# Kernel tuning notes

Measured on AMD Instinct MI355X. Metric: run time of the kernel, lower is better.

Reference implementation:

```python
import jax, jax.numpy as jnp
import numpy as np

B, P, ENC = 64, 196, 2048
ATT, DEC, EMB = 512, 512, 512
V, MAXLEN = 10000, 30


def setup_inputs() -> dict:
    key = jax.random.key(0)
    ks = jax.random.split(key, 20)
    s = 0.02
    inp = {
        "encoder_out": jax.random.normal(ks[0], (B, P, ENC), jnp.float32),
        "captions": jax.random.randint(ks[1], (B, MAXLEN), 0, V).astype(jnp.int64),
        "caption_lengths": jax.random.randint(ks[2], (B,), 1, MAXLEN).astype(jnp.int64),
        # parameters (PyTorch Linear convention: y = x @ W.T + b)
        "emb_table": jax.random.uniform(ks[3], (V, EMB), jnp.float32, -0.1, 0.1),
        "W_enc_att": jax.random.normal(ks[4], (ATT, ENC), jnp.float32) * s,
        "b_enc_att": jnp.zeros((ATT,), jnp.float32),
        "W_dec_att": jax.random.normal(ks[5], (ATT, DEC), jnp.float32) * s,
        "b_dec_att": jnp.zeros((ATT,), jnp.float32),
        "w_full_att": jax.random.normal(ks[6], (1, ATT), jnp.float32) * s,
        "b_full_att": jnp.zeros((1,), jnp.float32),
        "W_ih": jax.random.normal(ks[7], (4 * DEC, EMB + ENC), jnp.float32) * s,
        "b_ih": jnp.zeros((4 * DEC,), jnp.float32),
        "W_hh": jax.random.normal(ks[8], (4 * DEC, DEC), jnp.float32) * s,
        "b_hh": jnp.zeros((4 * DEC,), jnp.float32),
        "W_init_h": jax.random.normal(ks[9], (DEC, ENC), jnp.float32) * s,
        "b_init_h": jnp.zeros((DEC,), jnp.float32),
        "W_init_c": jax.random.normal(ks[10], (DEC, ENC), jnp.float32) * s,
        "b_init_c": jnp.zeros((DEC,), jnp.float32),
        "W_fc": jax.random.uniform(ks[11], (V, DEC), jnp.float32, -0.1, 0.1),
        "b_fc": jnp.zeros((V,), jnp.float32),
    }
    return inp


def reference(encoder_out, captions, caption_lengths, emb_table,
              W_enc_att, b_enc_att, W_dec_att, b_dec_att,
              w_full_att, b_full_att, W_ih, b_ih, W_hh, b_hh,
              W_init_h, b_init_h, W_init_c, b_init_c, W_fc, b_fc):
    # init hidden state from mean-pooled encoder features
    mean_enc = encoder_out.mean(axis=1)                       # [B, ENC]
    h0 = mean_enc @ W_init_h.T + b_init_h                     # [B, DEC]
    c0 = mean_enc @ W_init_c.T + b_init_c                     # [B, DEC]

    # encoder-side attention projection is time-invariant: hoist out of the loop
    att1 = jnp.einsum('bpe,ae->bpa', encoder_out, W_enc_att) + b_enc_att  # [B, P, ATT]

    embeddings = emb_table[captions]                          # [B, T, EMB]
    T = captions.shape[1] - 1
    emb_steps = jnp.swapaxes(embeddings[:, :T, :], 0, 1)      # [T, B, EMB]

    def step(carry, emb_t):
        h, c = carry
        att2 = h @ W_dec_att.T + b_dec_att                    # [B, ATT]
        e = (jax.nn.relu(att1 + att2[:, None, :]) @ w_full_att.T + b_full_att)[..., 0]  # [B, P]
        alpha = jax.nn.softmax(e, axis=1)                     # [B, P]
        context = jnp.einsum('bp,bpe->be', alpha, encoder_out)  # [B, ENC]
        x = jnp.concatenate([emb_t, context], axis=1)         # [B, EMB+ENC]
        gates = x @ W_ih.T + b_ih + h @ W_hh.T + b_hh         # [B, 4*DEC]
        i, f, g, o = jnp.split(gates, 4, axis=1)
        c_new = jax.nn.sigmoid(f) * c + jax.nn.sigmoid(i) * jnp.tanh(g)
        h_new = jax.nn.sigmoid(o) * jnp.tanh(c_new)
        preds = h_new @ W_fc.T + b_fc                         # dropout in eval mode = identity
        return (h_new, c_new), (preds, alpha)

    _, (preds_seq, alpha_seq) = jax.lax.scan(step, (h0, c0), emb_steps)
    predictions = jnp.swapaxes(preds_seq, 0, 1)               # [B, T, V]
    alphas = jnp.swapaxes(alpha_seq, 0, 1)                    # [B, T, P]
    return predictions, alphas
```

## Files before the change

### kernel.cpp

```cpp
#include <hip/hip_runtime.h>
#include <cstddef>

constexpr int B_   = 64;
constexpr int P_   = 196;
constexpr int ENC_ = 2048;
constexpr int ATT_ = 512;
constexpr int DEC_ = 512;
constexpr int EMB_ = 512;
constexpr int V_   = 10000;
constexpr int MAXLEN_ = 30;
constexpr int T_   = 29;
constexpr int G4_  = 2048;
constexpr int KIH_ = 2560;
constexpr int XK2_ = 2560;

constexpr int NBLK = 256;
constexpr int TPB  = 1024;
constexpr int NT   = NBLK * TPB;
constexpr int NW   = NT / 64;
constexpr int FSTR = 16;
constexpr size_t ZS_ = (size_t)B_ * G4_;
constexpr int NPT = 625;

typedef __attribute__((ext_vector_type(8))) short short8;
typedef __attribute__((ext_vector_type(4))) float f32x4;
using us = unsigned short;

__device__ __forceinline__ us f2bf(float x) {
    union { float f; unsigned u; } v; v.f = x;
    unsigned r = v.u + 0x7fff + ((v.u >> 16) & 1);
    return (us)(r >> 16);
}
__device__ __forceinline__ float bf2f(us u) {
    union { unsigned u; float f; } v; v.u = ((unsigned)u) << 16;
    return v.f;
}

__device__ __forceinline__ unsigned ld4cc(const void* p) {
    unsigned r;
    asm volatile("global_load_dword %0, %1, off sc1\n\ts_waitcnt vmcnt(0)"
                 : "=v"(r) : "v"(p) : "memory");
    return r;
}
__device__ __forceinline__ void ld4cc_x8(const float* p0, const float* p1,
                                         const float* p2, const float* p3,
                                         const float* p4, const float* p5,
                                         const float* p6, const float* p7,
                                         float* o) {
    float r0, r1, r2, r3, r4, r5, r6, r7;
    asm volatile("global_load_dword %0, %8, off sc1\n\t"
                 "global_load_dword %1, %9, off sc1\n\t"
                 "global_load_dword %2, %10, off sc1\n\t"
                 "global_load_dword %3, %11, off sc1\n\t"
                 "global_load_dword %4, %12, off sc1\n\t"
                 "global_load_dword %5, %13, off sc1\n\t"
                 "global_load_dword %6, %14, off sc1\n\t"
                 "global_load_dword %7, %15, off sc1\n\t"
                 "s_waitcnt vmcnt(0)"
                 : "=&v"(r0), "=&v"(r1), "=&v"(r2), "=&v"(r3),
                   "=&v"(r4), "=&v"(r5), "=&v"(r6), "=&v"(r7)
                 : "v"(p0), "v"(p1), "v"(p2), "v"(p3),
                   "v"(p4), "v"(p5), "v"(p6), "v"(p7) : "memory");
    o[0]=r0; o[1]=r1; o[2]=r2; o[3]=r3; o[4]=r4; o[5]=r5; o[6]=r6; o[7]=r7;
}
__device__ __forceinline__ void ld16cc_x3(const void* p0, const void* p1, const void* p2,
                                          short8* a, short8* b, short8* c) {
    short8 ra, rb, rc;
    asm volatile("global_load_dwordx4 %0, %3, off sc1\n\t"
                 "global_load_dwordx4 %1, %4, off sc1\n\t"
                 "global_load_dwordx4 %2, %5, off sc1\n\t"
                 "s_waitcnt vmcnt(0)"
                 : "=&v"(ra), "=&v"(rb), "=&v"(rc)
                 : "v"(p0), "v"(p1), "v"(p2) : "memory");
    *a = ra; *b = rb; *c = rc;
}
__device__ __forceinline__ void ld16cc_x4(const void* p0, const void* p1,
                                          const void* p2, const void* p3,
                                          short8* a, short8* b, short8* c, short8* d) {
    short8 ra, rb, rc, rd;
    asm volatile("global_load_dwordx4 %0, %4, off sc1\n\t"
                 "global_load_dwordx4 %1, %5, off sc1\n\t"
                 "global_load_dwordx4 %2, %6, off sc1\n\t"
                 "global_load_dwordx4 %3, %7, off sc1\n\t"
                 "s_waitcnt vmcnt(0)"
                 : "=&v"(ra), "=&v"(rb), "=&v"(rc), "=&v"(rd)
                 : "v"(p0), "v"(p1), "v"(p2), "v"(p3) : "memory");
    *a = ra; *b = rb; *c = rc; *d = rd;
}
__device__ __forceinline__ void ldf8cc(const void* p0, const void* p1, f32x4* a, f32x4* b) {
    f32x4 ra, rb;
    asm volatile("global_load_dwordx4 %0, %2, off sc1\n\t"
                 "global_load_dwordx4 %1, %3, off sc1\n\t"
                 "s_waitcnt vmcnt(0)"
                 : "=&v"(ra), "=&v"(rb) : "v"(p0), "v"(p1) : "memory");
    *a = ra; *b = rb;
}
__device__ __forceinline__ void st4cc(void* p, unsigned v) {
    asm volatile("global_store_dword %0, %1, off sc1" :: "v"(p), "v"(v) : "memory");
}
__device__ __forceinline__ void st2cc(void* p, unsigned v) {
    asm volatile("global_store_short %0, %1, off sc1" :: "v"(p), "v"(v) : "memory");
}
__device__ __forceinline__ float wredsum(float a) {
#pragma unroll
    for (int o = 32; o > 0; o >>= 1) a += __shfl_xor(a, o);
    return a;
}

template<bool REL>
__device__ __forceinline__ void gbar_arrive(unsigned* flags, unsigned tok) {
    asm volatile("s_waitcnt vmcnt(0)" ::: "memory");
    __syncthreads();
    if (threadIdx.x == 0)
        __hip_atomic_store(&flags[blockIdx.x * FSTR], tok,
                           REL ? __ATOMIC_RELEASE : __ATOMIC_RELAXED,
                           __HIP_MEMORY_SCOPE_AGENT);
}
__device__ __forceinline__ void gbar_wait(unsigned* flags, unsigned tok) {
    if (threadIdx.x < NBLK) {
        while (__hip_atomic_load(&flags[threadIdx.x * FSTR], __ATOMIC_RELAXED,
                                 __HIP_MEMORY_SCOPE_AGENT) < tok)
            __builtin_amdgcn_s_sleep(1);
    }
    __syncthreads();
}
template<bool REL>
__device__ __forceinline__ void gbar(unsigned* flags, unsigned tok) {
    gbar_arrive<REL>(flags, tok);
    gbar_wait(flags, tok);
}

__device__ __forceinline__ void cvt8(const float* __restrict__ src, us* __restrict__ dst) {
    const float4* p = (const float4*)src;
    float4 a = p[0], b = p[1];
    union { short8 v; us u[8]; } o;
    o.u[0] = f2bf(a.x); o.u[1] = f2bf(a.y); o.u[2] = f2bf(a.z); o.u[3] = f2bf(a.w);
    o.u[4] = f2bf(b.x); o.u[5] = f2bf(b.y); o.u[6] = f2bf(b.z); o.u[7] = f2bf(b.w);
    *(short8*)dst = o.v;
}

__device__ __forceinline__ float score8(short8 v, const f32x4& lo, const f32x4& hi,
                                        const float4& w0, const float4& w1) {
    float acc = 0.f, x;
    x = bf2f((us)v[0]) + lo[0]; acc += fmaxf(x, 0.f) * w0.x;
    x = bf2f((us)v[1]) + lo[1]; acc += fmaxf(x, 0.f) * w0.y;
    x = bf2f((us)v[2]) + lo[2]; acc += fmaxf(x, 0.f) * w0.z;
    x = bf2f((us)v[3]) + lo[3]; acc += fmaxf(x, 0.f) * w0.w;
    x = bf2f((us)v[4]) + hi[0]; acc += fmaxf(x, 0.f) * w1.x;
    x = bf2f((us)v[5]) + hi[1]; acc += fmaxf(x, 0.f) * w1.y;
    x = bf2f((us)v[6]) + hi[2]; acc += fmaxf(x, 0.f) * w1.z;
    x = bf2f((us)v[7]) + hi[3]; acc += fmaxf(x, 0.f) * w1.w;
    return acc;
}

__device__ __forceinline__ void preds_task(const us* s_h, const us* __restrict__ wfcb,
                                           const float* __restrict__ b_fc,
                                           float* __restrict__ outp,
                                           int nt, int tt, int lane) {
    const int r = lane & 15, g = lane >> 4;
    f32x4 acc[4] = {{0,0,0,0},{0,0,0,0},{0,0,0,0},{0,0,0,0}};
    const us* Brow = wfcb + (size_t)(nt*16 + r)*DEC_ + g*8;
    const us* As   = s_h + r*520 + g*8;
#pragma unroll
    for (int k0 = 0; k0 < DEC_; k0 += 64) {
        short8 b0 = *(const short8*)(Brow + k0);
        short8 b1 = *(const short8*)(Brow + k0 + 32);
#pragma unroll
        for (int mt = 0; mt < 4; ++mt) {
            short8 a0 = *(const short8*)(As + mt*16*520 + k0);
            short8 a1 = *(const short8*)(As + mt*16*520 + k0 + 32);
            acc[mt] = __builtin_amdgcn_mfma_f32_16x16x32_bf16(a0, b0, acc[mt], 0, 0, 0);
            acc[mt] = __builtin_amdgcn_mfma_f32_16x16x32_bf16(a1, b1, acc[mt], 0, 0, 0);
        }
    }
    const int n = nt*16 + r;
    const float bv = b_fc[n];
#pragma unroll
    for (int mt = 0; mt < 4; ++mt)
#pragma unroll
        for (int i = 0; i < 4; ++i) {
            int b = mt*16 + g*4 + i;
            outp[(size_t)b*(T_*V_) + (size_t)tt*V_ + n] = acc[mt][i] + bv;
        }
}

__global__ __launch_bounds__(TPB) void k_persist(
    const float* __restrict__ enc, const int* __restrict__ captions,
    const float* __restrict__ emb_table,
    const float* __restrict__ W_enc_att, const float* __restrict__ b_enc_att,
    const float* __restrict__ W_dec_att, const float* __restrict__ b_dec_att,
    const float* __restrict__ w_full,
    const float* __restrict__ W_ih, const float* __restrict__ b_ih,
    const float* __restrict__ W_hh, const float* __restrict__ b_hh,
    const float* __restrict__ W_init_h, const float* __restrict__ b_init_h,
    const float* __restrict__ W_init_c, const float* __restrict__ b_init_c,
    const float* __restrict__ W_fc, const float* __restrict__ b_fc,
    us* encb, us* wencb, us* wdecb, us* wfcb, us* wcat2, us* wembW,
    us* winitb, us* xembA, us* att1b, us* hbuf, us* xcatb, us* meanbb,
    float* cst, float* att2G, float* gp, float* gpe, float* bsum,
    unsigned* flags, float* outp, float* outa)
{
    __shared__ us s_stage[64 * 520];
    __shared__ us s_wb[64 * 328];
    __shared__ us s_wd[16 * 520];
    __shared__ float s_e[P_];
    __shared__ float s_al[P_];
    __shared__ float s_red[32];

    const int tid = threadIdx.x, bid = blockIdx.x;
    const int gtid = bid * TPB + tid;
    const int wid  = gtid >> 6;
    const int w    = tid >> 6;
    const int lane = tid & 63;
    unsigned tok = 0;
    float creg = 0.f;
    us* const hb0 = hbuf;
    us* const hb1 = hbuf + (size_t)B_ * DEC_;

    for (int i = gtid; i < B_*P_*ENC_/8; i += NT) cvt8(enc + (size_t)i*8, encb + (size_t)i*8);
    for (int i = gtid; i < ATT_*ENC_/8; i += NT) cvt8(W_enc_att + (size_t)i*8, wencb + (size_t)i*8);
    for (int i = gtid; i < ATT_*DEC_/8; i += NT) cvt8(W_dec_att + (size_t)i*8, wdecb + (size_t)i*8);
    for (int i = gtid; i < V_*DEC_/8;   i += NT) cvt8(W_fc + (size_t)i*8, wfcb + (size_t)i*8);
    for (int i = gtid; i < G4_*XK2_/8;  i += NT) {
        int n = (i*8) / XK2_, k = (i*8) % XK2_;
        const float* src = (k < ENC_) ? (W_ih + (size_t)n*KIH_ + EMB_ + k)
                                      : (W_hh + (size_t)n*DEC_ + (k - ENC_));
        cvt8(src, wcat2 + (size_t)i*8);
    }
    for (int i = gtid; i < G4_*EMB_/8;  i += NT)
        cvt8(W_ih + ((size_t)((i*8) / EMB_))*KIH_ + ((i*8) % EMB_), wembW + (size_t)i*8);
    for (int i = gtid; i < 1024*ENC_/8; i += NT) {
        int n = (i*8) >> 11, k = (i*8) & (ENC_ - 1);
        const float* src = (n < 512) ? (W_init_h + (size_t)n*ENC_ + k)
                                     : (W_init_c + (size_t)(n-512)*ENC_ + k);
        cvt8(src, winitb + (size_t)i*8);
    }
    for (int i = gtid; i < T_*B_*EMB_/8; i += NT) {
        int r = i >> 6, c8 = i & 63;
        int t = r >> 6, b = r & 63;
        int cap = captions[b*MAXLEN_ + t];
        cvt8(emb_table + (size_t)cap*EMB_ + c8*8, xembA + (size_t)r*EMB_ + c8*8);
    }
    if (gtid < G4_) bsum[gtid] = b_ih[gtid] + b_hh[gtid];
    if (gtid < B_*ENC_) {
        int b = gtid >> 11, e = gtid & (ENC_ - 1);
        const float* base = enc + (size_t)b*P_*ENC_ + e;
        float s = 0.f;
        for (int p = 0; p < P_; ++p) s += base[(size_t)p*ENC_];
        meanbb[gtid] = f2bf(s * (1.f / P_));
    }
    gbar<true>(flags, ++tok);

    for (int task = wid; task < 256 + 1856; task += NW) {
        const int r = lane & 15, g = lane >> 4;
        if (task < 256) {
            const int mt = task & 3, nt = task >> 2;
            const int m0 = mt*16, n0 = nt*16;
            const us* Ar = meanbb + (size_t)(m0 + r)*ENC_ + g*8;
            const us* Br = winitb + (size_t)(n0 + r)*ENC_ + g*8;
            f32x4 acc0 = {0,0,0,0}, acc1 = {0,0,0,0};
#pragma unroll 4
            for (int k0 = 0; k0 < ENC_; k0 += 64) {
                acc0 = __builtin_amdgcn_mfma_f32_16x16x32_bf16(
                    *(const short8*)(Ar + k0), *(const short8*)(Br + k0), acc0, 0, 0, 0);
                acc1 = __builtin_amdgcn_mfma_f32_16x16x32_bf16(
                    *(const short8*)(Ar + k0 + 32), *(const short8*)(Br + k0 + 32), acc1, 0, 0, 0);
            }
            const int n = n0 + r;
            if (n < 512) {
                float bv = b_init_h[n];
#pragma unroll
                for (int i = 0; i < 4; ++i) {
                    int b = m0 + g*4 + i;
                    unsigned hv = f2bf(acc0[i] + acc1[i] + bv);
                    st2cc(hb1 + b*DEC_ + n, hv);
                    st2cc(xcatb + (size_t)b*XK2_ + ENC_ + n, hv);
                }
            } else {
                int d = n - 512;
                float bv = b_init_c[d];
#pragma unroll
                for (int i = 0; i < 4; ++i)
                    st4cc(cst + (m0 + g*4 + i)*DEC_ + d,
                          __float_as_uint(acc0[i] + acc1[i] + bv));
            }
        } else {
            const int q = task - 256;
            const int m0 = (q >> 6) * 64, n0 = (q & 63) * 32;
            f32x4 acc[4][2] = {};
            const us* Ab = xembA + (size_t)(m0 + r)*EMB_ + g*8;
            const us* Bb = wembW + (size_t)(n0 + r)*EMB_ + g*8;
#pragma unroll 2
            for (int k0 = 0; k0 < EMB_; k0 += 32) {
                short8 af[4], bfr[2];
#pragma unroll
                for (int mi = 0; mi < 4; ++mi)
                    af[mi] = *(const short8*)(Ab + (size_t)mi*16*EMB_ + k0);
#pragma unroll
                for (int nj = 0; nj < 2; ++nj)
                    bfr[nj] = *(const short8*)(Bb + (size_t)nj*16*EMB_ + k0);
#pragma unroll
                for (int mi = 0; mi < 4; ++mi)
#pragma unroll
                    for (int nj = 0; nj < 2; ++nj)
                        acc[mi][nj] = __builtin_amdgcn_mfma_f32_16x16x32_bf16(
                            af[mi], bfr[nj], acc[mi][nj], 0, 0, 0);
            }
#pragma unroll
            for (int mi = 0; mi < 4; ++mi)
#pragma unroll
                for (int nj = 0; nj < 2; ++nj) {
                    int n = n0 + nj*16 + r;
                    float bv = bsum[n];
#pragma unroll
                    for (int i = 0; i < 4; ++i) {
                        int m = m0 + mi*16 + g*4 + i;
                        gpe[(size_t)m*G4_ + n] = acc[mi][nj][i] + bv;
                    }
                }
        }
    }
    gbar<true>(flags, ++tok);

    for (int task = wid; task < 3264; task += NW) {
        const int r = lane & 15, g = lane >> 4;
        if (task < 3136) {
            int mt = task >> 4, nt2 = task & 15;
            int m0 = mt*64, n0 = nt2*32;
            f32x4 acc[4][2] = {};
            const us* Ab = encb + (size_t)(m0 + r)*ENC_ + g*8;
            const us* Bb = wencb + (size_t)(n0 + r)*ENC_ + g*8;
#pragma unroll 2
            for (int k0 = 0; k0 < ENC_; k0 += 32) {
                short8 af[4], bfr[2];
#pragma unroll
                for (int mi = 0; mi < 4; ++mi)
                    af[mi] = *(const short8*)(Ab + (size_t)mi*16*ENC_ + k0);
#pragma unroll
                for (int nj = 0; nj < 2; ++nj)
                    bfr[nj] = *(const short8*)(Bb + (size_t)nj*16*ENC_ + k0);
#pragma unroll
                for (int mi = 0; mi < 4; ++mi)
#pragma unroll
                    for (int nj = 0; nj < 2; ++nj)
                        acc[mi][nj] = __builtin_amdgcn_mfma_f32_16x16x32_bf16(
                            af[mi], bfr[nj], acc[mi][nj], 0, 0, 0);
            }
#pragma unroll
            for (int mi = 0; mi < 4; ++mi)
#pragma unroll
                for (int nj = 0; nj < 2; ++nj) {
                    int n = n0 + nj*16 + r;
                    float bv = b_enc_att[n];
#pragma unroll
                    for (int i = 0; i < 4; ++i) {
                        int m = m0 + mi*16 + g*4 + i;
                        att1b[(size_t)m*ATT_ + n] = f2bf(acc[mi][nj][i] + bv);
                    }
                }
        } else {
            int q = task - 3136;
            int nt = q >> 2, mt = q & 3;
            const us* Ar = hb1 + (size_t)(mt*16 + r)*DEC_ + g*8;
            const us* Br = wdecb + (size_t)(nt*16 + r)*DEC_ + g*8;
            f32x4 acc0 = {0,0,0,0}, acc1 = {0,0,0,0};
#pragma unroll 4
            for (int k0 = 0; k0 < DEC_; k0 += 64) {
                short8 a0, a1, dum;
                ld16cc_x3(Ar + k0, Ar + k0 + 32, Ar + k0, &a0, &a1, &dum);
                acc0 = __builtin_amdgcn_mfma_f32_16x16x32_bf16(
                    a0, *(const short8*)(Br + k0), acc0, 0, 0, 0);
                acc1 = __builtin_amdgcn_mfma_f32_16x16x32_bf16(
                    a1, *(const short8*)(Br + k0 + 32), acc1, 0, 0, 0);
            }
            int n = nt*16 + r;
            float bv = b_dec_att[n];
#pragma unroll
            for (int i = 0; i < 4; ++i)
                st4cc(att2G + (size_t)(mt*16 + g*4 + i)*ATT_ + n,
                      __float_as_uint(acc0[i] + acc1[i] + bv));
        }
    }
    gbar<true>(flags, ++tok);

    {
        const int z = bid >> 5, nb = bid & 31;
        for (int c = tid; c < 2560; c += TPB) {
            int row = c / 40, col8 = c % 40;
            *(short8*)(s_wb + row*328 + col8*8) =
                *(const short8*)(wcat2 + (size_t)(nb*64 + row)*XK2_ + (size_t)z*320 + col8*8);
        }
        if (bid < 32)
            for (int c = tid; c < 1024; c += TPB) {
                int row = c >> 6, col8 = c & 63;
                *(short8*)(s_wd + row*520 + col8*8) =
                    *(const short8*)(wdecb + (size_t)(bid*16 + row)*DEC_ + col8*8);
            }
        if (tid < 128) creg = __uint_as_float(ld4cc(cst + bid*128 + tid));
        __syncthreads();
    }

    for (int t = 0; t < T_; ++t) {
        {
            const int b = bid & 63, cc = bid >> 6;
            f32x4 a2lo, a2hi;
            const float* ap = att2G + (size_t)b*ATT_ + lane*8;
            ldf8cc(ap, ap + 4, &a2lo, &a2hi);
            const float4 w0 = *(const float4*)(w_full + lane*8);
            const float4 w1 = *(const float4*)(w_full + lane*8 + 4);
            const us* a1base = att1b + (size_t)b*P_*ATT_ + lane*8;
            for (int p = w; p < P_; p += 32) {
                const int p2 = p + 16;
                short8 v0 = *(const short8*)(a1base + (size_t)p*ATT_);
                short8 v1 = (p2 < P_) ? *(const short8*)(a1base + (size_t)p2*ATT_) : v0;
                float acc0 = score8(v0, a2lo, a2hi, w0, w1);
                float acc1 = score8(v1, a2lo, a2hi, w0, w1);
                acc0 = wredsum(acc0);
                acc1 = wredsum(acc1);
                if (lane == 0) {
                    s_e[p] = acc0;
                    if (p2 < P_) s_e[p2] = acc1;
                }
            }
            __syncthreads();
            float v = (tid < P_) ? s_e[tid] : -3.4e38f;
            float mx = v;
#pragma unroll
            for (int o = 32; o > 0; o >>= 1) mx = fmaxf(mx, __shfl_xor(mx, o));
            if (lane == 0) s_red[w] = mx;
            __syncthreads();
            mx = s_red[0];
#pragma unroll
            for (int j = 1; j < 16; ++j) mx = fmaxf(mx, s_red[j]);
            float ev = (tid < P_) ? expf(v - mx) : 0.f;
            float sm = wredsum(ev);
            if (lane == 0) s_red[16 + w] = sm;
            __syncthreads();
            float tot = 0.f;
#pragma unroll
            for (int j = 0; j < 16; ++j) tot += s_red[16 + j];
            if (tid < P_) {
                float al = ev / tot;
                s_al[tid] = al;
                if (cc == 0) outa[((size_t)b*T_ + t)*P_ + tid] = al;
            }
            __syncthreads();
            float a[8] = {};
            const us* ep = encb + (size_t)b*P_*ENC_ + cc*512 + lane*8;
            for (int p = w; p < P_; p += 16) {
                short8 vv = *(const short8*)(ep + (size_t)p*ENC_);
                float al = s_al[p];
#pragma unroll
                for (int j = 0; j < 8; ++j) a[j] += al * bf2f((us)vv[j]);
            }
            float* s_accf = (float*)s_stage;
            {
                f32x4 lo = {a[0],a[1],a[2],a[3]}, hi = {a[4],a[5],a[6],a[7]};
                *(f32x4*)(s_accf + w*512 + lane*8)     = lo;
                *(f32x4*)(s_accf + w*512 + lane*8 + 4) = hi;
            }
            __syncthreads();
            if (tid < 256) {
                int c2 = tid*2;
                float s0 = 0.f, s1 = 0.f;
#pragma unroll
                for (int q = 0; q < 16; ++q) {
                    s0 += s_accf[q*512 + c2];
                    s1 += s_accf[q*512 + c2 + 1];
                }
                unsigned pk = (unsigned)f2bf(s0) | ((unsigned)f2bf(s1) << 16);
                st4cc(xcatb + (size_t)b*XK2_ + cc*512 + c2, pk);
            }
            __syncthreads();
        }
        gbar<false>(flags, ++tok);

        {
            const int z = bid >> 5;
            {
                short8 v0, v1, v2;
                int c0 = tid, c1 = tid + 1024, c2i = tid + 2048;
                const us* p0 = xcatb + (size_t)(c0/40)*XK2_ + z*320 + (c0%40)*8;
                const us* p1 = xcatb + (size_t)(c1/40)*XK2_ + z*320 + (c1%40)*8;
                bool has2 = c2i < 2560;
                const us* p2 = has2 ? xcatb + (size_t)(c2i/40)*XK2_ + z*320 + (c2i%40)*8 : p0;
                ld16cc_x3(p0, p1, p2, &v0, &v1, &v2);
                *(short8*)(s_stage + (c0/40)*328 + (c0%40)*8) = v0;
                *(short8*)(s_stage + (c1/40)*328 + (c1%40)*8) = v1;
                if (has2) *(short8*)(s_stage + (c2i/40)*328 + (c2i%40)*8) = v2;
            }
            __syncthreads();
            const int nt = (bid & 31)*4 + (w >> 2), mt = w & 3;
            const int r = lane & 15, g = lane >> 4;
            const us* sxr = s_stage + (mt*16 + r)*328 + g*8;
            const us* Br  = s_wb + ((w >> 2)*16 + r)*328 + g*8;
            f32x4 acc0 = {0,0,0,0}, acc1 = {0,0,0,0};
#pragma unroll
            for (int k0 = 0; k0 < 320; k0 += 64) {
                acc0 = __builtin_amdgcn_mfma_f32_16x16x32_bf16(
                    *(const short8*)(sxr + k0), *(const short8*)(Br + k0), acc0, 0, 0, 0);
                acc1 = __builtin_amdgcn_mfma_f32_16x16x32_bf16(
                    *(const short8*)(sxr + k0 + 32), *(const short8*)(Br + k0 + 32), acc1, 0, 0, 0);
            }
            const int n = nt*16 + r;
#pragma unroll
            for (int i = 0; i < 4; ++i) {
                int m = mt*16 + g*4 + i;
                st4cc(gp + ZS_*z + (size_t)m*G4_ + n, __float_as_uint(acc0[i] + acc1[i]));
            }
            __syncthreads();
        }
        gbar<false>(flags, ++tok);

        {
            float* sg = (float*)s_stage;
            if (tid < 512) {
                const int cell = tid & 127, gate = tid >> 7;
                const int idx = bid*128 + cell;
                const int b = idx >> 9, d = idx & 511;
                const float* gz = gp + (size_t)b*G4_ + gate*512 + d;
                float vz[8];
                ld4cc_x8(gz, gz + ZS_, gz + 2*ZS_, gz + 3*ZS_,
                         gz + 4*ZS_, gz + 5*ZS_, gz + 6*ZS_, gz + 7*ZS_, vz);
                sg[tid] = ((vz[0]+vz[1]) + (vz[2]+vz[3])) + ((vz[4]+vz[5]) + (vz[6]+vz[7]));
            }
            __syncthreads();
            if (tid < 128) {
                const int idx = bid*128 + tid;
                const int b = idx >> 9, d = idx & 511;
                const float* ge = gpe + ((size_t)(t*B_ + b))*G4_ + d;
                float gi = sg[tid]       + ge[0];
                float gf = sg[128 + tid] + ge[512];
                float gg = sg[256 + tid] + ge[1024];
                float go = sg[384 + tid] + ge[1536];
                float si = 1.f / (1.f + expf(-gi));
                float sf = 1.f / (1.f + expf(-gf));
                float so = 1.f / (1.f + expf(-go));
                float cn = sf * creg + si * tanhf(gg);
                creg = cn;
                float hn = so * tanhf(cn);
                unsigned hv = f2bf(hn);
                us* hnew = (t & 1) ? hb1 : hb0;
                st2cc(hnew + idx, hv);
                st2cc(xcatb + (size_t)b*XK2_ + ENC_ + d, hv);
            }
        }
        gbar<false>(flags, ++tok);

        if (t != T_ - 1) {
            ++tok;
            if (bid < 32) {
                {
                    const us* hbn = (t & 1) ? hb1 : hb0;
                    short8 v0, v1, v2, v3;
                    int c0 = tid, c1 = tid + 1024, c2i = tid + 2048, c3 = tid + 3072;
                    ld16cc_x4(hbn + (c0>>6)*DEC_ + (c0&63)*8, hbn + (c1>>6)*DEC_ + (c1&63)*8,
                              hbn + (c2i>>6)*DEC_ + (c2i&63)*8, hbn + (c3>>6)*DEC_ + (c3&63)*8,
                              &v0, &v1, &v2, &v3);
                    *(short8*)(s_stage + (c0>>6)*520 + (c0&63)*8) = v0;
                    *(short8*)(s_stage + (c1>>6)*520 + (c1&63)*8) = v1;
                    *(short8*)(s_stage + (c2i>>6)*520 + (c2i&63)*8) = v2;
                    *(short8*)(s_stage + (c3>>6)*520 + (c3&63)*8) = v3;
                }
                __syncthreads();
                if (w < 4) {
                    const int r = lane & 15, g = lane >> 4;
                    const us* As = s_stage + (w*16 + r)*520 + g*8;
                    const us* Bs = s_wd + r*520 + g*8;
                    f32x4 acc0 = {0,0,0,0}, acc1 = {0,0,0,0};
#pragma unroll
                    for (int k0 = 0; k0 < DEC_; k0 += 64) {
                        acc0 = __builtin_amdgcn_mfma_f32_16x16x32_bf16(
                            *(const short8*)(As + k0), *(const short8*)(Bs + k0), acc0, 0, 0, 0);
                        acc1 = __builtin_amdgcn_mfma_f32_16x16x32_bf16(
                            *(const short8*)(As + k0 + 32), *(const short8*)(Bs + k0 + 32), acc1, 0, 0, 0);
                    }
                    const int n = bid*16 + r;
                    float bv = b_dec_att[n];
#pragma unroll
                    for (int i = 0; i < 4; ++i)
                        st4cc(att2G + (size_t)(w*16 + g*4 + i)*ATT_ + n,
                              __float_as_uint(acc0[i] + acc1[i] + bv));
                }
                gbar_arrive<false>(flags, tok);
                gbar_wait(flags, tok);
            } else {
                gbar_arrive<false>(flags, tok);
                if (t > 0) {
                    const us* hbo = (t & 1) ? hb0 : hb1;
                    short8 v0, v1, v2, v3;
                    int c0 = tid, c1 = tid + 1024, c2i = tid + 2048, c3 = tid + 3072;
                    ld16cc_x4(hbo + (c0>>6)*DEC_ + (c0&63)*8, hbo + (c1>>6)*DEC_ + (c1&63)*8,
                              hbo + (c2i>>6)*DEC_ + (c2i&63)*8, hbo + (c3>>6)*DEC_ + (c3&63)*8,
                              &v0, &v1, &v2, &v3);
                    *(short8*)(s_stage + (c0>>6)*520 + (c0&63)*8) = v0;
                    *(short8*)(s_stage + (c1>>6)*520 + (c1&63)*8) = v1;
                    *(short8*)(s_stage + (c2i>>6)*520 + (c2i&63)*8) = v2;
                    *(short8*)(s_stage + (c3>>6)*520 + (c3&63)*8) = v3;
                    __syncthreads();
                    const int tq = (bid - 32)*3 + w;
                    if (w < 3 && tq < NPT)
                        preds_task(s_stage, wfcb, b_fc, outp, tq, t - 1, lane);
                }
                gbar_wait(flags, tok);
            }
        } else {
            if (bid >= 32) {
                const us* hbo = (t & 1) ? hb0 : hb1;
                short8 v0, v1, v2, v3;
                int c0 = tid, c1 = tid + 1024, c2i = tid + 2048, c3 = tid + 3072;
                ld16cc_x4(hbo + (c0>>6)*DEC_ + (c0&63)*8, hbo + (c1>>6)*DEC_ + (c1&63)*8,
                          hbo + (c2i>>6)*DEC_ + (c2i&63)*8, hbo + (c3>>6)*DEC_ + (c3&63)*8,
                          &v0, &v1, &v2, &v3);
                *(short8*)(s_stage + (c0>>6)*520 + (c0&63)*8) = v0;
                *(short8*)(s_stage + (c1>>6)*520 + (c1&63)*8) = v1;
                *(short8*)(s_stage + (c2i>>6)*520 + (c2i&63)*8) = v2;
                *(short8*)(s_stage + (c3>>6)*520 + (c3&63)*8) = v3;
                __syncthreads();
                const int tq = (bid - 32)*3 + w;
                if (w < 3 && tq < NPT)
                    preds_task(s_stage, wfcb, b_fc, outp, tq, t - 1, lane);
            }
        }
    }

    if (bid < 40) {
        __syncthreads();
        const us* hbn = ((T_ - 1) & 1) ? hb1 : hb0;
        {
            short8 v0, v1, v2, v3;
            int c0 = tid, c1 = tid + 1024, c2i = tid + 2048, c3 = tid + 3072;
            ld16cc_x4(hbn + (c0>>6)*DEC_ + (c0&63)*8, hbn + (c1>>6)*DEC_ + (c1&63)*8,
                      hbn + (c2i>>6)*DEC_ + (c2i&63)*8, hbn + (c3>>6)*DEC_ + (c3&63)*8,
                      &v0, &v1, &v2, &v3);
            *(short8*)(s_stage + (c0>>6)*520 + (c0&63)*8) = v0;
            *(short8*)(s_stage + (c1>>6)*520 + (c1&63)*8) = v1;
            *(short8*)(s_stage + (c2i>>6)*520 + (c2i&63)*8) = v2;
            *(short8*)(s_stage + (c3>>6)*520 + (c3&63)*8) = v3;
        }
        __syncthreads();
        const int tq = bid*16 + w;
        if (tq < NPT)
            preds_task(s_stage, wfcb, b_fc, outp, tq, T_ - 1, lane);
    }
}

extern "C" void kernel_launch(void* const* d_in, const int* in_sizes, int n_in,
                              void* d_out, int out_size, void* d_ws, size_t ws_size,
                              hipStream_t stream) {
    const float* enc       = (const float*)d_in[0];
    const int*   captions  = (const int*)d_in[1];
    const float* emb_table = (const float*)d_in[3];
    const float* W_enc_att = (const float*)d_in[4];
    const float* b_enc_att = (const float*)d_in[5];
    const float* W_dec_att = (const float*)d_in[6];
    const float* b_dec_att = (const float*)d_in[7];
    const float* w_full    = (const float*)d_in[8];
    const float* W_ih      = (const float*)d_in[10];
    const float* b_ih      = (const float*)d_in[11];
    const float* W_hh      = (const float*)d_in[12];
    const float* b_hh      = (const float*)d_in[13];
    const float* W_init_h  = (const float*)d_in[14];
    const float* b_init_h  = (const float*)d_in[15];
    const float* W_init_c  = (const float*)d_in[16];
    const float* b_init_c  = (const float*)d_in[17];
    const float* W_fc      = (const float*)d_in[18];
    const float* b_fc      = (const float*)d_in[19];

    char* ws = (char*)d_ws;
    size_t off = 0;
    auto alloc = [&](size_t bytes) {
        void* p = ws + off;
        off = (off + bytes + 255) & ~(size_t)255;
        return p;
    };
    us* encb   = (us*)alloc((size_t)B_ * P_ * ENC_ * 2);
    us* wencb  = (us*)alloc((size_t)ATT_ * ENC_ * 2);
    us* wdecb  = (us*)alloc((size_t)ATT_ * DEC_ * 2);
    us* wfcb   = (us*)alloc((size_t)V_ * DEC_ * 2);
    us* wcat2  = (us*)alloc((size_t)G4_ * XK2_ * 2);
    us* wembW  = (us*)alloc((size_t)G4_ * EMB_ * 2);
    us* winitb = (us*)alloc((size_t)1024 * ENC_ * 2);
    us* xembA  = (us*)alloc((size_t)T_ * B_ * EMB_ * 2);
    us* att1b  = (us*)alloc((size_t)B_ * P_ * ATT_ * 2);
    us* hbuf   = (us*)alloc((size_t)2 * B_ * DEC_ * 2);
    us* xcatb  = (us*)alloc((size_t)B_ * XK2_ * 2);
    us* meanbb = (us*)alloc((size_t)B_ * ENC_ * 2);
    float* cst   = (float*)alloc((size_t)B_ * DEC_ * 4);
    float* att2G = (float*)alloc((size_t)B_ * ATT_ * 4);
    float* gp    = (float*)alloc((size_t)B_ * G4_ * 8 * 4);
    float* gpe   = (float*)alloc((size_t)T_ * B_ * G4_ * 4);
    float* bsum  = (float*)alloc((size_t)G4_ * 4);
    unsigned* flags = (unsigned*)alloc((size_t)(NBLK + 1) * FSTR * 4);

    float* outp = (float*)d_out;
    float* outa = outp + (size_t)B_ * T_ * V_;

    hipMemsetAsync(flags, 0, (NBLK + 1) * FSTR * sizeof(unsigned), stream);
    k_persist<<<NBLK, TPB, 0, stream>>>(
        enc, captions, emb_table, W_enc_att, b_enc_att, W_dec_att, b_dec_att,
        w_full, W_ih, b_ih, W_hh, b_hh, W_init_h, b_init_h, W_init_c, b_init_c,
        W_fc, b_fc,
        encb, wencb, wdecb, wfcb, wcat2, wembW, winitb, xembA, att1b, hbuf, xcatb,
        meanbb, cst, att2G, gp, gpe, bsum, flags, outp, outa);
}
```

Measured before the change: 1.204 ms.

## Fuse LSTM gate GEMM with cell update per block, dropping a grid barrier

Reorders the gate-weight rows so each of 128 blocks owns 4 hidden units across all four gates over the full K. That lets a block finish its gate GEMM, reduce it through shared memory and apply the LSTM cell update without the global split-K partial buffer and its extra grid barrier. The prediction GEMM moves onto the other 128 blocks and runs concurrently with the gate step, so fewer blocks do the recurrent work. A-operands are now loaded straight from global memory into registers, and the full 16x2560 weight slice stays resident in LDS.

Measured after the change: 1.573 ms. 1.31x slower.

```diff
diff --git a/kernel.cpp b/kernel.cpp
--- a/kernel.cpp
+++ b/kernel.cpp
@@ -19,7 +19,6 @@
 constexpr int NT   = NBLK * TPB;
 constexpr int NW   = NT / 64;
 constexpr int FSTR = 16;
-constexpr size_t ZS_ = (size_t)B_ * G4_;
 constexpr int NPT = 625;
 
 typedef __attribute__((ext_vector_type(8))) short short8;
@@ -41,27 +40,6 @@
     asm volatile("global_load_dword %0, %1, off sc1\n\ts_waitcnt vmcnt(0)"
                  : "=v"(r) : "v"(p) : "memory");
     return r;
-}
-__device__ __forceinline__ void ld4cc_x8(const float* p0, const float* p1,
-                                         const float* p2, const float* p3,
-                                         const float* p4, const float* p5,
-                                         const float* p6, const float* p7,
-                                         float* o) {
-    float r0, r1, r2, r3, r4, r5, r6, r7;
-    asm volatile("global_load_dword %0, %8, off sc1\n\t"
-                 "global_load_dword %1, %9, off sc1\n\t"
-                 "global_load_dword %2, %10, off sc1\n\t"
-                 "global_load_dword %3, %11, off sc1\n\t"
-                 "global_load_dword %4, %12, off sc1\n\t"
-                 "global_load_dword %5, %13, off sc1\n\t"
-                 "global_load_dword %6, %14, off sc1\n\t"
-                 "global_load_dword %7, %15, off sc1\n\t"
-                 "s_waitcnt vmcnt(0)"
-                 : "=&v"(r0), "=&v"(r1), "=&v"(r2), "=&v"(r3),
-                   "=&v"(r4), "=&v"(r5), "=&v"(r6), "=&v"(r7)
-                 : "v"(p0), "v"(p1), "v"(p2), "v"(p3),
-                   "v"(p4), "v"(p5), "v"(p6), "v"(p7) : "memory");
-    o[0]=r0; o[1]=r1; o[2]=r2; o[3]=r3; o[4]=r4; o[5]=r5; o[6]=r6; o[7]=r7;
 }
 __device__ __forceinline__ void ld16cc_x3(const void* p0, const void* p1, const void* p2,
                                           short8* a, short8* b, short8* c) {
@@ -108,26 +86,19 @@
 }
 
 template<bool REL>
-__device__ __forceinline__ void gbar_arrive(unsigned* flags, unsigned tok) {
+__device__ __forceinline__ void gbar(unsigned* flags, unsigned tok) {
     asm volatile("s_waitcnt vmcnt(0)" ::: "memory");
     __syncthreads();
     if (threadIdx.x == 0)
         __hip_atomic_store(&flags[blockIdx.x * FSTR], tok,
                            REL ? __ATOMIC_RELEASE : __ATOMIC_RELAXED,
                            __HIP_MEMORY_SCOPE_AGENT);
-}
-__device__ __forceinline__ void gbar_wait(unsigned* flags, unsigned tok) {
     if (threadIdx.x < NBLK) {
         while (__hip_atomic_load(&flags[threadIdx.x * FSTR], __ATOMIC_RELAXED,
                                  __HIP_MEMORY_SCOPE_AGENT) < tok)
             __builtin_amdgcn_s_sleep(1);
     }
     __syncthreads();
-}
-template<bool REL>
-__device__ __forceinline__ void gbar(unsigned* flags, unsigned tok) {
-    gbar_arrive<REL>(flags, tok);
-    gbar_wait(flags, tok);
 }
 
 __device__ __forceinline__ void cvt8(const float* __restrict__ src, us* __restrict__ dst) {
@@ -197,12 +168,11 @@
     const float* __restrict__ W_fc, const float* __restrict__ b_fc,
     us* encb, us* wencb, us* wdecb, us* wfcb, us* wcat2, us* wembW,
     us* winitb, us* xembA, us* att1b, us* hbuf, us* xcatb, us* meanbb,
-    float* cst, float* att2G, float* gp, float* gpe, float* bsum,
+    float* cst, float* att2G, float* gpe, float* bsum,
     unsigned* flags, float* outp, float* outa)
 {
     __shared__ us s_stage[64 * 520];
-    __shared__ us s_wb[64 * 328];
-    __shared__ us s_wd[16 * 520];
+    __shared__ us s_w[16 * 2568];
     __shared__ float s_e[P_];
     __shared__ float s_al[P_];
     __shared__ float s_red[32];
@@ -222,7 +192,9 @@
     for (int i = gtid; i < ATT_*DEC_/8; i += NT) cvt8(W_dec_att + (size_t)i*8, wdecb + (size_t)i*8);
     for (int i = gtid; i < V_*DEC_/8;   i += NT) cvt8(W_fc + (size_t)i*8, wfcb + (size_t)i*8);
     for (int i = gtid; i < G4_*XK2_/8;  i += NT) {
-        int n = (i*8) / XK2_, k = (i*8) % XK2_;
+        int rr = (i*8) / XK2_, k = (i*8) % XK2_;
+        int j = rr & 15, kblk = rr >> 4;
+        int n = (j >> 2)*512 + kblk*4 + (j & 3);
         const float* src = (k < ENC_) ? (W_ih + (size_t)n*KIH_ + EMB_ + k)
                                       : (W_hh + (size_t)n*DEC_ + (k - ENC_));
         cvt8(src, wcat2 + (size_t)i*8);
@@ -383,22 +355,25 @@
     }
     gbar<true>(flags, ++tok);
 
-    {
-        const int z = bid >> 5, nb = bid & 31;
-        for (int c = tid; c < 2560; c += TPB) {
-            int row = c / 40, col8 = c % 40;
-            *(short8*)(s_wb + row*328 + col8*8) =
-                *(const short8*)(wcat2 + (size_t)(nb*64 + row)*XK2_ + (size_t)z*320 + col8*8);
-        }
-        if (bid < 32)
-            for (int c = tid; c < 1024; c += TPB) {
-                int row = c >> 6, col8 = c & 63;
-                *(short8*)(s_wd + row*520 + col8*8) =
-                    *(const short8*)(wdecb + (size_t)(bid*16 + row)*DEC_ + col8*8);
-            }
-        if (tid < 128) creg = __uint_as_float(ld4cc(cst + bid*128 + tid));
-        __syncthreads();
-    }
+    if (bid >= 128) {
+        const int kblk = bid - 128;
+        for (int c = tid; c < 16*320; c += TPB) {
+            int row = c / 320, col8 = c % 320;
+            *(short8*)(s_w + row*2568 + col8*8) =
+                *(const short8*)(wcat2 + (size_t)(kblk*16 + row)*XK2_ + col8*8);
+        }
+        if (tid < 256) {
+            int b = tid >> 2, dj = tid & 3;
+            creg = __uint_as_float(ld4cc(cst + b*DEC_ + kblk*4 + dj));
+        }
+    } else if (bid < 32) {
+        for (int c = tid; c < 1024; c += TPB) {
+            int row = c >> 6, col8 = c & 63;
+            *(short8*)(s_w + row*520 + col8*8) =
+                *(const short8*)(wdecb + (size_t)(bid*16 + row)*DEC_ + col8*8);
+        }
+    }
+    __syncthreads();
 
     for (int t = 0; t < T_; ++t) {
         {
@@ -475,64 +450,49 @@
         }
         gbar<false>(flags, ++tok);
 
-        {
-            const int z = bid >> 5;
-            {
-                short8 v0, v1, v2;
-                int c0 = tid, c1 = tid + 1024, c2i = tid + 2048;
-                const us* p0 = xcatb + (size_t)(c0/40)*XK2_ + z*320 + (c0%40)*8;
-                const us* p1 = xcatb + (size_t)(c1/40)*XK2_ + z*320 + (c1%40)*8;
-                bool has2 = c2i < 2560;
-                const us* p2 = has2 ? xcatb + (size_t)(c2i/40)*XK2_ + z*320 + (c2i%40)*8 : p0;
-                ld16cc_x3(p0, p1, p2, &v0, &v1, &v2);
-                *(short8*)(s_stage + (c0/40)*328 + (c0%40)*8) = v0;
-                *(short8*)(s_stage + (c1/40)*328 + (c1%40)*8) = v1;
-                if (has2) *(short8*)(s_stage + (c2i/40)*328 + (c2i%40)*8) = v2;
-            }
-            __syncthreads();
-            const int nt = (bid & 31)*4 + (w >> 2), mt = w & 3;
+        if (bid >= 128) {
+            const int kblk = bid - 128;
             const int r = lane & 15, g = lane >> 4;
-            const us* sxr = s_stage + (mt*16 + r)*328 + g*8;
-            const us* Br  = s_wb + ((w >> 2)*16 + r)*328 + g*8;
+            const int mg = w & 3, kg = w >> 2;
+            const us* Abase = xcatb + (size_t)(mg*16 + r)*XK2_ + kg*640 + g*8;
+            short8 a[20];
+#pragma unroll
+            for (int i = 0; i < 20; ++i)
+                asm volatile("global_load_dwordx4 %0, %1, off sc1"
+                             : "=v"(a[i]) : "v"(Abase + i*32) : "memory");
+            asm volatile("s_waitcnt vmcnt(0)" ::: "memory");
+            __builtin_amdgcn_sched_barrier(0);
+            const us* Bb = s_w + r*2568 + kg*640 + g*8;
             f32x4 acc0 = {0,0,0,0}, acc1 = {0,0,0,0};
 #pragma unroll
-            for (int k0 = 0; k0 < 320; k0 += 64) {
+            for (int i = 0; i < 10; ++i) {
                 acc0 = __builtin_amdgcn_mfma_f32_16x16x32_bf16(
-                    *(const short8*)(sxr + k0), *(const short8*)(Br + k0), acc0, 0, 0, 0);
+                    a[2*i], *(const short8*)(Bb + i*64), acc0, 0, 0, 0);
                 acc1 = __builtin_amdgcn_mfma_f32_16x16x32_bf16(
-                    *(const short8*)(sxr + k0 + 32), *(const short8*)(Br + k0 + 32), acc1, 0, 0, 0);
-            }
-            const int n = nt*16 + r;
-#pragma unroll
-            for (int i = 0; i < 4; ++i) {
-                int m = mt*16 + g*4 + i;
-                st4cc(gp + ZS_*z + (size_t)m*G4_ + n, __float_as_uint(acc0[i] + acc1[i]));
-            }
-            __syncthreads();
-        }
-        gbar<false>(flags, ++tok);
-
-        {
-            float* sg = (float*)s_stage;
-            if (tid < 512) {
-                const int cell = tid & 127, gate = tid >> 7;
-                const int idx = bid*128 + cell;
-                const int b = idx >> 9, d = idx & 511;
-                const float* gz = gp + (size_t)b*G4_ + gate*512 + d;
-                float vz[8];
-                ld4cc_x8(gz, gz + ZS_, gz + 2*ZS_, gz + 3*ZS_,
-                         gz + 4*ZS_, gz + 5*ZS_, gz + 6*ZS_, gz + 7*ZS_, vz);
-                sg[tid] = ((vz[0]+vz[1]) + (vz[2]+vz[3])) + ((vz[4]+vz[5]) + (vz[6]+vz[7]));
-            }
-            __syncthreads();
-            if (tid < 128) {
-                const int idx = bid*128 + tid;
-                const int b = idx >> 9, d = idx & 511;
-                const float* ge = gpe + ((size_t)(t*B_ + b))*G4_ + d;
-                float gi = sg[tid]       + ge[0];
-                float gf = sg[128 + tid] + ge[512];
-                float gg = sg[256 + tid] + ge[1024];
-                float go = sg[384 + tid] + ge[1536];
+                    a[2*i+1], *(const short8*)(Bb + i*64 + 32), acc1, 0, 0, 0);
+            }
+            float* s_red4 = (float*)s_stage;
+            *(f32x4*)(s_red4 + ((kg*4 + mg)*64 + lane)*4) = acc0 + acc1;
+            __syncthreads();
+            if (tid < 256) {
+                const int b = tid >> 2, dj = tid & 3;
+                const int d = kblk*4 + dj;
+                const int mg2 = b >> 4, g2i = (b & 15) >> 2, ii = b & 3;
+                float gv[4];
+#pragma unroll
+                for (int g2 = 0; g2 < 4; ++g2) {
+                    const int ln = g2i*16 + (g2*4 + dj);
+                    float s = 0.f;
+#pragma unroll
+                    for (int kk = 0; kk < 4; ++kk)
+                        s += s_red4[((kk*4 + mg2)*64 + ln)*4 + ii];
+                    gv[g2] = s;
+                }
+                const float* geb = gpe + ((size_t)(t*B_ + b))*G4_ + d;
+                float gi = gv[0] + geb[0];
+                float gf = gv[1] + geb[512];
+                float gg = gv[2] + geb[1024];
+                float go = gv[3] + geb[1536];
                 float si = 1.f / (1.f + expf(-gi));
                 float sf = 1.f / (1.f + expf(-gf));
                 float so = 1.f / (1.f + expf(-go));
@@ -541,91 +501,65 @@
                 float hn = so * tanhf(cn);
                 unsigned hv = f2bf(hn);
                 us* hnew = (t & 1) ? hb1 : hb0;
-                st2cc(hnew + idx, hv);
+                st2cc(hnew + b*DEC_ + d, hv);
                 st2cc(xcatb + (size_t)b*XK2_ + ENC_ + d, hv);
             }
+        } else if (t > 0) {
+            const us* hbo = (t & 1) ? hb0 : hb1;
+            short8 v0, v1, v2, v3;
+            int c0 = tid, c1 = tid + 1024, c2i = tid + 2048, c3 = tid + 3072;
+            ld16cc_x4(hbo + (c0>>6)*DEC_ + (c0&63)*8, hbo + (c1>>6)*DEC_ + (c1&63)*8,
+                      hbo + (c2i>>6)*DEC_ + (c2i&63)*8, hbo + (c3>>6)*DEC_ + (c3&63)*8,
+                      &v0, &v1, &v2, &v3);
+            *(short8*)(s_stage + (c0>>6)*520 + (c0&63)*8) = v0;
+            *(short8*)(s_stage + (c1>>6)*520 + (c1&63)*8) = v1;
+            *(short8*)(s_stage + (c2i>>6)*520 + (c2i&63)*8) = v2;
+            *(short8*)(s_stage + (c3>>6)*520 + (c3&63)*8) = v3;
+            __syncthreads();
+            const int tq = bid*5 + w;
+            if (w < 5 && tq < NPT)
+                preds_task(s_stage, wfcb, b_fc, outp, tq, t - 1, lane);
         }
         gbar<false>(flags, ++tok);
-
-        if (t != T_ - 1) {
-            ++tok;
-            if (bid < 32) {
-                {
-                    const us* hbn = (t & 1) ? hb1 : hb0;
-                    short8 v0, v1, v2, v3;
-                    int c0 = tid, c1 = tid + 1024, c2i = tid + 2048, c3 = tid + 3072;
-                    ld16cc_x4(hbn + (c0>>6)*DEC_ + (c0&63)*8, hbn + (c1>>6)*DEC_ + (c1&63)*8,
-                              hbn + (c2i>>6)*DEC_ + (c2i&63)*8, hbn + (c3>>6)*DEC_ + (c3&63)*8,
-                              &v0, &v1, &v2, &v3);
-                    *(short8*)(s_stage + (c0>>6)*520 + (c0&63)*8) = v0;
-                    *(short8*)(s_stage + (c1>>6)*520 + (c1&63)*8) = v1;
-                    *(short8*)(s_stage + (c2i>>6)*520 + (c2i&63)*8) = v2;
-                    *(short8*)(s_stage + (c3>>6)*520 + (c3&63)*8) = v3;
+        if (t == T_ - 1) break;
+
+        if (bid < 32) {
+            const us* hbn = (t & 1) ? hb1 : hb0;
+            short8 v0, v1, v2, v3;
+            int c0 = tid, c1 = tid + 1024, c2i = tid + 2048, c3 = tid + 3072;
+            ld16cc_x4(hbn + (c0>>6)*DEC_ + (c0&63)*8, hbn + (c1>>6)*DEC_ + (c1&63)*8,
+                      hbn + (c2i>>6)*DEC_ + (c2i&63)*8, hbn + (c3>>6)*DEC_ + (c3&63)*8,
+                      &v0, &v1, &v2, &v3);
+            *(short8*)(s_stage + (c0>>6)*520 + (c0&63)*8) = v0;
+            *(short8*)(s_stage + (c1>>6)*520 + (c1&63)*8) = v1;
+            *(short8*)(s_stage + (c2i>>6)*520 + (c2i&63)*8) = v2;
+            *(short8*)(s_stage + (c3>>6)*520 + (c3&63)*8) = v3;
+            __syncthreads();
+            if (w < 4) {
+                const int r = lane & 15, g = lane >> 4;
+                const us* As = s_stage + (w*16 + r)*520 + g*8;
+                const us* Bs = s_w + r*520 + g*8;
+                f32x4 acc0 = {0,0,0,0}, acc1 = {0,0,0,0};
+#pragma unroll
+                for (int k0 = 0; k0 < DEC_; k0 += 64) {
+                    acc0 = __builtin_amdgcn_mfma_f32_16x16x32_bf16(
+                        *(const short8*)(As + k0), *(const short8*)(Bs + k0), acc0, 0, 0, 0);
+                    acc1 = __builtin_amdgcn_mfma_f32_16x16x32_bf16(
+                        *(const short8*)(As + k0 + 32), *(const short8*)(Bs + k0 + 32), acc1, 0, 0, 0);
                 }
-                __syncthreads();
-                if (w < 4) {
-                    const int r = lane & 15, g = lane >> 4;
-                    const us* As = s_stage + (w*16 + r)*520 + g*8;
-                    const us* Bs = s_wd + r*520 + g*8;
-                    f32x4 acc0 = {0,0,0,0}, acc1 = {0,0,0,0};
-#pragma unroll
-                    for (int k0 = 0; k0 < DEC_; k0 += 64) {
-                        acc0 = __builtin_amdgcn_mfma_f32_16x16x32_bf16(
-                            *(const short8*)(As + k0), *(const short8*)(Bs + k0), acc0, 0, 0, 0);
-                        acc1 = __builtin_amdgcn_mfma_f32_16x16x32_bf16(
-                            *(const short8*)(As + k0 + 32), *(const short8*)(Bs + k0 + 32), acc1, 0, 0, 0);
-                    }
-                    const int n = bid*16 + r;
-                    float bv = b_dec_att[n];
-#pragma unroll
-                    for (int i = 0; i < 4; ++i)
-                        st4cc(att2G + (size_t)(w*16 + g*4 + i)*ATT_ + n,
-                              __float_as_uint(acc0[i] + acc1[i] + bv));
-                }
-                gbar_arrive<false>(flags, tok);
-                gbar_wait(flags, tok);
-            } else {
-                gbar_arrive<false>(flags, tok);
-                if (t > 0) {
-                    const us* hbo = (t & 1) ? hb0 : hb1;
-                    short8 v0, v1, v2, v3;
-                    int c0 = tid, c1 = tid + 1024, c2i = tid + 2048, c3 = tid + 3072;
-                    ld16cc_x4(hbo + (c0>>6)*DEC_ + (c0&63)*8, hbo + (c1>>6)*DEC_ + (c1&63)*8,
-                              hbo + (c2i>>6)*DEC_ + (c2i&63)*8, hbo + (c3>>6)*DEC_ + (c3&63)*8,
-                              &v0, &v1, &v2, &v3);
-                    *(short8*)(s_stage + (c0>>6)*520 + (c0&63)*8) = v0;
-                    *(short8*)(s_stage + (c1>>6)*520 + (c1&63)*8) = v1;
-                    *(short8*)(s_stage + (c2i>>6)*520 + (c2i&63)*8) = v2;
-                    *(short8*)(s_stage + (c3>>6)*520 + (c3&63)*8) = v3;
-                    __syncthreads();
-                    const int tq = (bid - 32)*3 + w;
-                    if (w < 3 && tq < NPT)
-                        preds_task(s_stage, wfcb, b_fc, outp, tq, t - 1, lane);
-                }
-                gbar_wait(flags, tok);
-            }
-        } else {
-            if (bid >= 32) {
-                const us* hbo = (t & 1) ? hb0 : hb1;
-                short8 v0, v1, v2, v3;
-                int c0 = tid, c1 = tid + 1024, c2i = tid + 2048, c3 = tid + 3072;
-                ld16cc_x4(hbo + (c0>>6)*DEC_ + (c0&63)*8, hbo + (c1>>6)*DEC_ + (c1&63)*8,
-                          hbo + (c2i>>6)*DEC_ + (c2i&63)*8, hbo + (c3>>6)*DEC_ + (c3&63)*8,
-                          &v0, &v1, &v2, &v3);
-                *(short8*)(s_stage + (c0>>6)*520 + (c0&63)*8) = v0;
-                *(short8*)(s_stage + (c1>>6)*520 + (c1&63)*8) = v1;
-                *(short8*)(s_stage + (c2i>>6)*520 + (c2i&63)*8) = v2;
-                *(short8*)(s_stage + (c3>>6)*520 + (c3&63)*8) = v3;
-                __syncthreads();
-                const int tq = (bid - 32)*3 + w;
-                if (w < 3 && tq < NPT)
-                    preds_task(s_stage, wfcb, b_fc, outp, tq, t - 1, lane);
-            }
-        }
+                const int n = bid*16 + r;
+                float bv = b_dec_att[n];
+#pragma unroll
+                for (int i = 0; i < 4; ++i)
+                    st4cc(att2G + (size_t)(w*16 + g*4 + i)*ATT_ + n,
+                          __float_as_uint(acc0[i] + acc1[i] + bv));
+            }
+            __syncthreads();
+        }
+        gbar<false>(flags, ++tok);
     }
 
     if (bid < 40) {
-        __syncthreads();
         const us* hbn = ((T_ - 1) & 1) ? hb1 : hb0;
         {
             short8 v0, v1, v2, v3;
@@ -688,7 +622,6 @@
     us* meanbb = (us*)alloc((size_t)B_ * ENC_ * 2);
     float* cst   = (float*)alloc((size_t)B_ * DEC_ * 4);
     float* att2G = (float*)alloc((size_t)B_ * ATT_ * 4);
-    float* gp    = (float*)alloc((size_t)B_ * G4_ * 8 * 4);
     float* gpe   = (float*)alloc((size_t)T_ * B_ * G4_ * 4);
     float* bsum  = (float*)alloc((size_t)G4_ * 4);
     unsigned* flags = (unsigned*)alloc((size_t)(NBLK + 1) * FSTR * 4);
@@ -702,5 +635,5 @@
         w_full, W_ih, b_ih, W_hh, b_hh, W_init_h, b_init_h, W_init_c, b_init_c,
         W_fc, b_fc,
         encb, wencb, wdecb, wfcb, wcat2, wembW, winitb, xembA, att1b, hbuf, xcatb,
-        meanbb, cst, att2G, gp, gpe, bsum, flags, outp, outa);
-}
+        meanbb, cst, att2G, gpe, bsum, flags, outp, outa);
+}
```
